# Performance work log

Measured on AMD Instinct MI355X. Metric: run time of the kernel, lower is better.

The kernel has to match this reference:

```python
import jax, jax.numpy as jnp
import numpy as np

B, S, T = 4096, 2048, 2  # batch of conversations, turns per conversation, num_tags


def setup_inputs() -> dict:
    key = jax.random.key(0)
    k1, k2, k3, k4, k5, k6 = jax.random.split(key, 6)
    emissions = jax.random.normal(k1, (B, S, T), dtype=jnp.float32)
    # learned transition matrices for DistanceCRF branch order:
    # [even2odd, I0, D_consecutive, D_nonconsecutive]
    trans_params = jax.random.normal(k2, (4, T, T), dtype=jnp.float32) * 0.1
    tags = jax.random.randint(k3, (B, S), 0, T)
    who2who = jax.random.randint(k4, (B, S), 0, 2)
    intime = jax.random.randint(k5, (B, S), 0, 3)
    distance = jax.random.randint(k6, (B, S), 0, 4)
    return {"emissions": emissions, "trans_params": trans_params, "tags": tags,
            "who2who": who2who, "intime": intime, "distance": distance}


def _select_trans(trans_params, who2who, intime, distance):
    """Per-step transition matrix selection (DistanceCRF logic).
    Returns [B, S, T, T]."""
    Tn = trans_params.shape[-1]
    # index 0 = zero 'padding' matrix (who2who == -1 case)
    bank = jnp.concatenate([jnp.zeros((1, Tn, Tn), trans_params.dtype), trans_params], axis=0)
    sel = jnp.where(who2who == -1, 0,
          jnp.where(who2who == 1, 1,          # even2odd
          jnp.where(intime == 0, 2,           # I0
          jnp.where(distance == 0, 3, 4))))   # D_consecutive / D_nonconsecutive
    return bank[sel]


def reference(emissions, trans_params, tags, who2who, intime, distance):
    Bn, Sn, Tn = emissions.shape
    trans = _select_trans(trans_params, who2who, intime, distance)  # [B,S,T,T]

    # ---- gold path score ----
    em_gold = jnp.take_along_axis(emissions, tags[..., None], axis=-1)[..., 0].sum(-1)  # [B]
    oh_prev = jax.nn.one_hot(tags[:, :-1], Tn, dtype=emissions.dtype)  # [B,S-1,T]
    oh_cur = jax.nn.one_hot(tags[:, 1:], Tn, dtype=emissions.dtype)
    tr_gold = jnp.einsum('bsij,bsi,bsj->b', trans[:, 1:], oh_prev, oh_cur)  # [B]
    gold_score = em_gold + tr_gold

    # ---- log partition via forward recursion (note: transition added at t=0 too,
    # matching the original implementation) ----
    def step(alpha, xs):
        em_t, tr_t = xs  # [B,T], [B,T,T]
        new_alpha = jax.nn.logsumexp(alpha[:, :, None] + em_t[:, None, :] + tr_t, axis=1)
        return new_alpha, None

    alpha0 = jnp.zeros((Bn, Tn), emissions.dtype)
    xs = (jnp.swapaxes(emissions, 0, 1), jnp.swapaxes(trans, 0, 1))  # [S,B,T], [S,B,T,T]
    alpha, _ = jax.lax.scan(step, alpha0, xs)
    total_score = jax.nn.logsumexp(alpha, axis=-1)  # [B]

    return jnp.stack([gold_score, total_score])  # [2, B]
```

## Files before the change

### kernel.cpp

```cpp
#include <hip/hip_runtime.h>
#include <math.h>

#define Bn 4096
#define Sn 2048
#define BLOCK 256
#define CHUNK (Sn / BLOCK)

__global__ __launch_bounds__(BLOCK) void crf_fwd(
    const float* __restrict__ emissions,
    const float* __restrict__ trans_params,
    const int*   __restrict__ tags,
    const int*   __restrict__ who2who,
    const int*   __restrict__ intime,
    const int*   __restrict__ distance,
    float*       __restrict__ out)
{
    const int b  = blockIdx.x;
    const int t  = threadIdx.x;
    const long base = (long)b * Sn;
    const int s0 = t * CHUNK;

    __shared__ __align__(16) float lbank[20];
    __shared__ __align__(16) float ebank[20];
    __shared__ float wm[4][6];

    if (t < 20) {
        float v = (t < 4) ? 0.0f : trans_params[t - 4];
        lbank[t] = v;
        ebank[t] = __expf(v);
    }
    __syncthreads();

    const int4* tp = (const int4*)(tags     + base) + t * 2;
    const int4* wp = (const int4*)(who2who  + base) + t * 2;
    const int4* ip = (const int4*)(intime   + base) + t * 2;
    const int4* dp = (const int4*)(distance + base) + t * 2;
    int4 ta = tp[0], tb = tp[1];
    int4 wa = wp[0], wb = wp[1];
    int4 ia = ip[0], ib = ip[1];
    int4 da = dp[0], db = dp[1];

    const float4* ep = (const float4*)(emissions + base * 2) + t * 4;
    float4 e0 = ep[0], e1 = ep[1], e2 = ep[2], e3 = ep[3];

    int tagv[CHUNK] = {ta.x, ta.y, ta.z, ta.w, tb.x, tb.y, tb.z, tb.w};
    int wv[CHUNK]   = {wa.x, wa.y, wa.z, wa.w, wb.x, wb.y, wb.z, wb.w};
    int iv[CHUNK]   = {ia.x, ia.y, ia.z, ia.w, ib.x, ib.y, ib.z, ib.w};
    int dv[CHUNK]   = {da.x, da.y, da.z, da.w, db.x, db.y, db.z, db.w};
    float emv[CHUNK][2] = {
        {e0.x, e0.y}, {e0.z, e0.w}, {e1.x, e1.y}, {e1.z, e1.w},
        {e2.x, e2.y}, {e2.z, e2.w}, {e3.x, e3.y}, {e3.z, e3.w}};

    int prev_tag = 0;
    if (t > 0) prev_tag = tags[base + s0 - 1];

    float m00, m01, m10, m11;
    float gold = 0.0f;

    #pragma unroll
    for (int k = 0; k < CHUNK; ++k) {
        int w = wv[k], it = iv[k], d = dv[k];
        int sel = (w == -1) ? 0 : (w == 1) ? 1 : (it == 0) ? 2 : (d == 0) ? 3 : 4;

        float4 P = *(const float4*)(ebank + sel * 4);
        float ek0 = emv[k][0], ek1 = emv[k][1];
        float x0 = __expf(ek0), x1 = __expf(ek1);

        if (k == 0) {
            m00 = P.x * x0; m01 = P.y * x1;
            m10 = P.z * x0; m11 = P.w * x1;
        } else {
            float n00 = fmaf(m00, P.x, m01 * P.z) * x0;
            float n01 = fmaf(m00, P.y, m01 * P.w) * x1;
            float n10 = fmaf(m10, P.x, m11 * P.z) * x0;
            float n11 = fmaf(m10, P.y, m11 * P.w) * x1;
            m00 = n00; m01 = n01; m10 = n10; m11 = n11;
        }

        int tg = tagv[k];
        gold += tg ? ek1 : ek0;
        if (k > 0 || t > 0) {
            int pt = (k == 0) ? prev_tag : tagv[k - 1];
            gold += lbank[(sel << 2) + (pt << 1) + tg];
        }
    }

    float mx  = fmaxf(fmaxf(m00, m01), fmaxf(m10, m11));
    float inv = 1.0f / mx;
    float L   = __logf(mx);
    m00 *= inv; m01 *= inv; m10 *= inv; m11 *= inv;

    #pragma unroll
    for (int m = 1; m < 64; m <<= 1) {
        float o00 = __shfl_xor(m00, m);
        float o01 = __shfl_xor(m01, m);
        float o10 = __shfl_xor(m10, m);
        float o11 = __shfl_xor(m11, m);
        float oL  = __shfl_xor(L, m);
        float og  = __shfl_xor(gold, m);
        bool up = (t & m) != 0;
        float a00 = up ? o00 : m00, a01 = up ? o01 : m01;
        float a10 = up ? o10 : m10, a11 = up ? o11 : m11;
        float b00 = up ? m00 : o00, b01 = up ? m01 : o01;
        float b10 = up ? m10 : o10, b11 = up ? m11 : o11;
        m00 = fmaf(a00, b00, a01 * b10);
        m01 = fmaf(a00, b01, a01 * b11);
        m10 = fmaf(a10, b00, a11 * b10);
        m11 = fmaf(a10, b01, a11 * b11);
        L += oL;
        gold += og;
    }

    int wave = t >> 6;
    if ((t & 63) == 0) {
        wm[wave][0] = m00; wm[wave][1] = m01;
        wm[wave][2] = m10; wm[wave][3] = m11;
        wm[wave][4] = L;   wm[wave][5] = gold;
    }
    __syncthreads();

    if (t == 0) {
        float r00 = wm[0][0], r01 = wm[0][1], r10 = wm[0][2], r11 = wm[0][3];
        float Ls = wm[0][4], g = wm[0][5];
        #pragma unroll
        for (int q = 1; q < 4; ++q) {
            float q00 = wm[q][0], q01 = wm[q][1], q10 = wm[q][2], q11 = wm[q][3];
            float n00 = fmaf(r00, q00, r01 * q10);
            float n01 = fmaf(r00, q01, r01 * q11);
            float n10 = fmaf(r10, q00, r11 * q10);
            float n11 = fmaf(r10, q01, r11 * q11);
            r00 = n00; r01 = n01; r10 = n10; r11 = n11;
            Ls += wm[q][4];
            g  += wm[q][5];
        }
        float tot = Ls + __logf(r00 + r01 + r10 + r11);
        out[b]      = g;
        out[Bn + b] = tot;
    }
}

extern "C" void kernel_launch(void* const* d_in, const int* in_sizes, int n_in,
                              void* d_out, int out_size, void* d_ws, size_t ws_size,
                              hipStream_t stream) {
    const float* emissions    = (const float*)d_in[0];
    const float* trans_params = (const float*)d_in[1];
    const int*   tags         = (const int*)d_in[2];
    const int*   who2who      = (const int*)d_in[3];
    const int*   intime       = (const int*)d_in[4];
    const int*   distance     = (const int*)d_in[5];
    float* out = (float*)d_out;

    crf_fwd<<<dim3(Bn), dim3(BLOCK), 0, stream>>>(
        emissions, trans_params, tags, who2who, intime, distance, out);
}
```

Measured before the change: 202.4 us.

## Use 1024-thread blocks with two steps per thread and shuffle-based cross-wave reduction

Raises the block to 1024 threads so each thread handles only two sequence steps instead of eight, shrinking the serial per-thread matrix chain and the register footprint. Global loads become int2/float4 per thread, and the previous tag comes from a lane shuffle. The final combine across 16 waves becomes a shuffle tree in wave 0 instead of a serial loop on one thread, with per-wave renormalisation before the combine. The cost is more work in the log-depth shuffle scans and larger blocks that may limit scheduling flexibility. The kernel stays memory-bound at roughly 100 MB read.

```diff
diff --git a/kernel.cpp b/kernel.cpp
--- a/kernel.cpp
+++ b/kernel.cpp
@@ -3,10 +3,9 @@
 
 #define Bn 4096
 #define Sn 2048
-#define BLOCK 256
-#define CHUNK (Sn / BLOCK)
+#define BLOCK 1024
 
-__global__ __launch_bounds__(BLOCK) void crf_fwd(
+__global__ __launch_bounds__(BLOCK) void crf_fused(
     const float* __restrict__ emissions,
     const float* __restrict__ trans_params,
     const int*   __restrict__ tags,
@@ -15,14 +14,23 @@
     const int*   __restrict__ distance,
     float*       __restrict__ out)
 {
-    const int b  = blockIdx.x;
-    const int t  = threadIdx.x;
+    const int b    = blockIdx.x;
+    const int t    = threadIdx.x;
+    const int lane = t & 63;
+    const int wave = t >> 6;
     const long base = (long)b * Sn;
-    const int s0 = t * CHUNK;
 
     __shared__ __align__(16) float lbank[20];
     __shared__ __align__(16) float ebank[20];
-    __shared__ float wm[4][6];
+    __shared__ float sred[16][8];
+
+    float4 e  = ((const float4*)(emissions + base * 2))[t];
+    int2   tg = ((const int2*)(tags     + base))[t];
+    int2   wh = ((const int2*)(who2who  + base))[t];
+    int2   it = ((const int2*)(intime   + base))[t];
+    int2   ds = ((const int2*)(distance + base))[t];
+    int ptag = 0;
+    if (lane == 0 && t > 0) ptag = tags[base + 2 * t - 1];
 
     if (t < 20) {
         float v = (t < 4) ? 0.0f : trans_params[t - 4];
@@ -31,59 +39,30 @@
     }
     __syncthreads();
 
-    const int4* tp = (const int4*)(tags     + base) + t * 2;
-    const int4* wp = (const int4*)(who2who  + base) + t * 2;
-    const int4* ip = (const int4*)(intime   + base) + t * 2;
-    const int4* dp = (const int4*)(distance + base) + t * 2;
-    int4 ta = tp[0], tb = tp[1];
-    int4 wa = wp[0], wb = wp[1];
-    int4 ia = ip[0], ib = ip[1];
-    int4 da = dp[0], db = dp[1];
+    int sel0 = (wh.x == -1) ? 0 : (wh.x == 1) ? 1
+             : (it.x == 0) ? 2 : (ds.x == 0) ? 3 : 4;
+    int sel1 = (wh.y == -1) ? 0 : (wh.y == 1) ? 1
+             : (it.y == 0) ? 2 : (ds.y == 0) ? 3 : 4;
+    float4 P0 = *(const float4*)(ebank + sel0 * 4);
+    float4 P1 = *(const float4*)(ebank + sel1 * 4);
+    float x00 = __expf(e.x), x01 = __expf(e.y);
+    float x10 = __expf(e.z), x11 = __expf(e.w);
 
-    const float4* ep = (const float4*)(emissions + base * 2) + t * 4;
-    float4 e0 = ep[0], e1 = ep[1], e2 = ep[2], e3 = ep[3];
+    float a00 = P0.x * x00, a01 = P0.y * x01;
+    float a10 = P0.z * x00, a11 = P0.w * x01;
+    float b00 = P1.x * x10, b01 = P1.y * x11;
+    float b10 = P1.z * x10, b11 = P1.w * x11;
+    float m00 = fmaf(a00, b00, a01 * b10);
+    float m01 = fmaf(a00, b01, a01 * b11);
+    float m10 = fmaf(a10, b00, a11 * b10);
+    float m11 = fmaf(a10, b01, a11 * b11);
 
-    int tagv[CHUNK] = {ta.x, ta.y, ta.z, ta.w, tb.x, tb.y, tb.z, tb.w};
-    int wv[CHUNK]   = {wa.x, wa.y, wa.z, wa.w, wb.x, wb.y, wb.z, wb.w};
-    int iv[CHUNK]   = {ia.x, ia.y, ia.z, ia.w, ib.x, ib.y, ib.z, ib.w};
-    int dv[CHUNK]   = {da.x, da.y, da.z, da.w, db.x, db.y, db.z, db.w};
-    float emv[CHUNK][2] = {
-        {e0.x, e0.y}, {e0.z, e0.w}, {e1.x, e1.y}, {e1.z, e1.w},
-        {e2.x, e2.y}, {e2.z, e2.w}, {e3.x, e3.y}, {e3.z, e3.w}};
-
-    int prev_tag = 0;
-    if (t > 0) prev_tag = tags[base + s0 - 1];
-
-    float m00, m01, m10, m11;
-    float gold = 0.0f;
-
-    #pragma unroll
-    for (int k = 0; k < CHUNK; ++k) {
-        int w = wv[k], it = iv[k], d = dv[k];
-        int sel = (w == -1) ? 0 : (w == 1) ? 1 : (it == 0) ? 2 : (d == 0) ? 3 : 4;
-
-        float4 P = *(const float4*)(ebank + sel * 4);
-        float ek0 = emv[k][0], ek1 = emv[k][1];
-        float x0 = __expf(ek0), x1 = __expf(ek1);
-
-        if (k == 0) {
-            m00 = P.x * x0; m01 = P.y * x1;
-            m10 = P.z * x0; m11 = P.w * x1;
-        } else {
-            float n00 = fmaf(m00, P.x, m01 * P.z) * x0;
-            float n01 = fmaf(m00, P.y, m01 * P.w) * x1;
-            float n10 = fmaf(m10, P.x, m11 * P.z) * x0;
-            float n11 = fmaf(m10, P.y, m11 * P.w) * x1;
-            m00 = n00; m01 = n01; m10 = n10; m11 = n11;
-        }
-
-        int tg = tagv[k];
-        gold += tg ? ek1 : ek0;
-        if (k > 0 || t > 0) {
-            int pt = (k == 0) ? prev_tag : tagv[k - 1];
-            gold += lbank[(sel << 2) + (pt << 1) + tg];
-        }
-    }
+    float gold = (tg.x ? e.y : e.x) + (tg.y ? e.w : e.z);
+    int pt0 = __shfl_up(tg.y, 1);
+    if (lane == 0) pt0 = ptag;
+    if (t > 0)
+        gold += lbank[(sel0 << 2) + (pt0 << 1) + tg.x];
+    gold += lbank[(sel1 << 2) + (tg.x << 1) + tg.y];
 
     float mx  = fmaxf(fmaxf(m00, m01), fmaxf(m10, m11));
     float inv = 1.0f / mx;
@@ -98,44 +77,60 @@
         float o11 = __shfl_xor(m11, m);
         float oL  = __shfl_xor(L, m);
         float og  = __shfl_xor(gold, m);
-        bool up = (t & m) != 0;
-        float a00 = up ? o00 : m00, a01 = up ? o01 : m01;
-        float a10 = up ? o10 : m10, a11 = up ? o11 : m11;
-        float b00 = up ? m00 : o00, b01 = up ? m01 : o01;
-        float b10 = up ? m10 : o10, b11 = up ? m11 : o11;
-        m00 = fmaf(a00, b00, a01 * b10);
-        m01 = fmaf(a00, b01, a01 * b11);
-        m10 = fmaf(a10, b00, a11 * b10);
-        m11 = fmaf(a10, b01, a11 * b11);
+        bool up = (lane & m) != 0;
+        float p00 = up ? o00 : m00, p01 = up ? o01 : m01;
+        float p10 = up ? o10 : m10, p11 = up ? o11 : m11;
+        float q00 = up ? m00 : o00, q01 = up ? m01 : o01;
+        float q10 = up ? m10 : o10, q11 = up ? m11 : o11;
+        m00 = fmaf(p00, q00, p01 * q10);
+        m01 = fmaf(p00, q01, p01 * q11);
+        m10 = fmaf(p10, q00, p11 * q10);
+        m11 = fmaf(p10, q01, p11 * q11);
         L += oL;
         gold += og;
     }
 
-    int wave = t >> 6;
-    if ((t & 63) == 0) {
-        wm[wave][0] = m00; wm[wave][1] = m01;
-        wm[wave][2] = m10; wm[wave][3] = m11;
-        wm[wave][4] = L;   wm[wave][5] = gold;
+    if (lane == 0) {
+        float mx2  = fmaxf(fmaxf(m00, m01), fmaxf(m10, m11));
+        float inv2 = 1.0f / mx2;
+        sred[wave][0] = m00 * inv2;
+        sred[wave][1] = m01 * inv2;
+        sred[wave][2] = m10 * inv2;
+        sred[wave][3] = m11 * inv2;
+        sred[wave][4] = L + __logf(mx2);
+        sred[wave][5] = gold;
     }
     __syncthreads();
 
-    if (t == 0) {
-        float r00 = wm[0][0], r01 = wm[0][1], r10 = wm[0][2], r11 = wm[0][3];
-        float Ls = wm[0][4], g = wm[0][5];
+    if (wave == 0 && lane < 16) {
+        float r00 = sred[lane][0], r01 = sred[lane][1];
+        float r10 = sred[lane][2], r11 = sred[lane][3];
+        float rL  = sred[lane][4], rg  = sred[lane][5];
         #pragma unroll
-        for (int q = 1; q < 4; ++q) {
-            float q00 = wm[q][0], q01 = wm[q][1], q10 = wm[q][2], q11 = wm[q][3];
-            float n00 = fmaf(r00, q00, r01 * q10);
-            float n01 = fmaf(r00, q01, r01 * q11);
-            float n10 = fmaf(r10, q00, r11 * q10);
-            float n11 = fmaf(r10, q01, r11 * q11);
-            r00 = n00; r01 = n01; r10 = n10; r11 = n11;
-            Ls += wm[q][4];
-            g  += wm[q][5];
+        for (int m = 1; m < 16; m <<= 1) {
+            float o00 = __shfl_xor(r00, m);
+            float o01 = __shfl_xor(r01, m);
+            float o10 = __shfl_xor(r10, m);
+            float o11 = __shfl_xor(r11, m);
+            float oL  = __shfl_xor(rL, m);
+            float og  = __shfl_xor(rg, m);
+            bool up = (lane & m) != 0;
+            float p00 = up ? o00 : r00, p01 = up ? o01 : r01;
+            float p10 = up ? o10 : r10, p11 = up ? o11 : r11;
+            float q00 = up ? r00 : o00, q01 = up ? r01 : o01;
+            float q10 = up ? r10 : o10, q11 = up ? r11 : o11;
+            r00 = fmaf(p00, q00, p01 * q10);
+            r01 = fmaf(p00, q01, p01 * q11);
+            r10 = fmaf(p10, q00, p11 * q10);
+            r11 = fmaf(p10, q01, p11 * q11);
+            rL += oL;
+            rg += og;
         }
-        float tot = Ls + __logf(r00 + r01 + r10 + r11);
-        out[b]      = g;
-        out[Bn + b] = tot;
+        if (lane == 0) {
+            float tot = rL + __logf(r00 + r01 + r10 + r11);
+            out[b]      = rg;
+            out[Bn + b] = tot;
+        }
     }
 }
 
@@ -150,6 +145,6 @@
     const int*   distance     = (const int*)d_in[5];
     float* out = (float*)d_out;
 
-    crf_fwd<<<dim3(Bn), dim3(BLOCK), 0, stream>>>(
+    crf_fused<<<dim3(Bn), dim3(BLOCK), 0, stream>>>(
         emissions, trans_params, tags, who2who, intime, distance, out);
 }
```

Result: no change. 199.7 us (-1.3%).
